# Performance work log

Measured on AMD Instinct MI355X. Metric: run time of the kernel, lower is better.

The kernel has to match this reference:

```python
import jax, jax.numpy as jnp
import numpy as np

B, S, V, K = 8, 128, 32000, 32


def setup_inputs() -> dict:
    key = jax.random.key(0)
    ks = jax.random.split(key, 8)
    return {
        "neural_logit": jax.random.normal(ks[0], (B, S, V), dtype=jnp.float32),
        "optor_vals": jax.random.randint(ks[1], (B, S, K), 0, V),
        "optor_dists": jax.random.uniform(ks[2], (B, S, K), dtype=jnp.float32) * 100.0,
        "const_vals": jax.random.randint(ks[3], (B, S, K), 0, V),
        "const_dists": jax.random.uniform(ks[4], (B, S, K), dtype=jnp.float32) * 100.0,
        "prev_words": jax.random.randint(ks[5], (B, S), 0, V),
        "optor_lamda": jnp.array([0.7], dtype=jnp.float32),
        "const_lamda": jnp.array([0.7], dtype=jnp.float32),
        "optor_temp": jnp.array([10.0], dtype=jnp.float32),
        "const_temp": jnp.array([10.0], dtype=jnp.float32),
    }


def _knn_prob(vals, dists, temp, vocab):
    # kernel-density: softmax over negative distances, scatter-add into vocab ids
    b, s, k = vals.shape
    w = jax.nn.softmax(-dists / temp, axis=-1)            # [B,S,K]
    rows = jnp.arange(b * s)[:, None]                     # [BS,1]
    p = jnp.zeros((b * s, vocab), w.dtype)
    p = p.at[rows, vals.reshape(b * s, k)].add(w.reshape(b * s, k))
    return p.reshape(b, s, vocab)


def reference(neural_logit, optor_vals, optor_dists, const_vals, const_dists,
              prev_words, optor_lamda, const_lamda, optor_temp, const_temp):
    nmt_prob = jax.nn.softmax(neural_logit, axis=-1)      # [B,S,V]

    optor_knn = _knn_prob(optor_vals, optor_dists, optor_temp[0], V)
    optor_combined = optor_lamda[0] * optor_knn + (1.0 - optor_lamda[0]) * nmt_prob

    const_knn = _knn_prob(const_vals, const_dists, const_temp[0], V)
    const_combined = const_lamda[0] * const_knn + (1.0 - const_lamda[0]) * nmt_prob

    pw = prev_words                                        # [B,S]
    optor_mask = (pw <= 88) | ((pw >= 91) & (pw <= 291))
    const_mask = (pw == 89) | (pw == 90) | (pw >= 292)

    combined = (optor_combined * optor_mask[:, :, None].astype(nmt_prob.dtype)
                + const_combined * const_mask[:, :, None].astype(nmt_prob.dtype))
    return combined
```

## Files before the change

kernel.cpp:

```cpp
#include <hip/hip_runtime.h>
#include <math.h>

constexpr int Bc = 8, Sc = 128, Vc = 32000, Kc = 32;
constexpr int NT = 1024;
constexpr int V4 = Vc / 4;
constexpr int ITERS = (V4 + NT - 1) / NT;
constexpr int NWAVES = NT / 64;

typedef float vfloat4 __attribute__((ext_vector_type(4)));

__global__ __launch_bounds__(NT) void SR_knnModel_kernel(
    const float* __restrict__ logit,
    const int*   __restrict__ optor_vals,
    const float* __restrict__ optor_dists,
    const int*   __restrict__ const_vals,
    const float* __restrict__ const_dists,
    const int*   __restrict__ prev_words,
    const float* __restrict__ optor_lamda,
    const float* __restrict__ const_lamda,
    const float* __restrict__ optor_temp,
    const float* __restrict__ const_temp,
    float* __restrict__ out)
{
    const int row = blockIdx.x;
    const int t   = threadIdx.x;
    const size_t base = (size_t)row * Vc;
    const float4* __restrict__ xin  = (const float4*)(logit + base);
    float* __restrict__        orow = out + base;

    float4 r[ITERS];
    float lmax = -INFINITY;
#pragma unroll
    for (int i = 0; i < ITERS; ++i) {
        const int idx = t + i * NT;
        if (i < ITERS - 1 || idx < V4) {
            const float4 v = xin[idx];
            r[i] = v;
            lmax = fmaxf(lmax, fmaxf(fmaxf(v.x, v.y), fmaxf(v.z, v.w)));
        }
    }

    float lsum = 0.f;
#pragma unroll
    for (int i = 0; i < ITERS; ++i) {
        const int idx = t + i * NT;
        if (i < ITERS - 1 || idx < V4) {
            float4 v = r[i];
            v.x = __expf(v.x - lmax);
            v.y = __expf(v.y - lmax);
            v.z = __expf(v.z - lmax);
            v.w = __expf(v.w - lmax);
            r[i] = v;
            lsum += (v.x + v.y) + (v.z + v.w);
        }
    }

    const int pw = prev_words[row];
    const float ol = optor_lamda[0];
    const float cl = const_lamda[0];

    float m = lmax, s = lsum;
#pragma unroll
    for (int off = 32; off > 0; off >>= 1) {
        const float om = __shfl_xor(m, off);
        const float os = __shfl_xor(s, off);
        const float M2 = fmaxf(m, om);
        s = s * __expf(m - M2) + os * __expf(om - M2);
        m = M2;
    }
    __shared__ float2 red[NWAVES];
    const int wave = t >> 6;
    if ((t & 63) == 0) red[wave] = make_float2(m, s);
    __syncthreads();
    float M = red[0].x, S = red[0].y;
#pragma unroll
    for (int w = 1; w < NWAVES; ++w) {
        const float2 p = red[w];
        const float nM = fmaxf(M, p.x);
        S = S * __expf(M - nM) + p.y * __expf(p.x - nM);
        M = nM;
    }

    const bool om_ = (pw <= 88) || (pw >= 91 && pw <= 291);
    const bool cm_ = (pw == 89) || (pw == 90) || (pw >= 292);
    const float omf = om_ ? 1.f : 0.f;
    const float cmf = cm_ ? 1.f : 0.f;
    const float cn = (1.f - ol) * omf + (1.f - cl) * cmf;
    const float f = __expf(lmax - M) * (cn / S);

#pragma unroll
    for (int i = 0; i < ITERS; ++i) {
        const int idx = t + i * NT;
        if (i < ITERS - 1 || idx < V4) {
            const float4 v = r[i];
            vfloat4 o;
            o.x = v.x * f; o.y = v.y * f; o.z = v.z * f; o.w = v.w * f;
            __builtin_nontemporal_store(o, (vfloat4*)orow + idx);
        }
    }
    __syncthreads();

    if (t < 32 || (t >= 64 && t < 96)) {
        const bool is_opt = (t < 32);
        const float scale = is_opt ? ol * omf : cl * cmf;
        if (scale != 0.f) {
            const int k = t & 31;
            const int*   vals  = is_opt ? optor_vals  : const_vals;
            const float* dists = is_opt ? optor_dists : const_dists;
            const float  temp  = is_opt ? optor_temp[0] : const_temp[0];
            const float sc = -dists[row * Kc + k] / temp;
            float mm = sc;
#pragma unroll
            for (int off = 16; off > 0; off >>= 1)
                mm = fmaxf(mm, __shfl_xor(mm, off));
            const float e = __expf(sc - mm);
            float sm = e;
#pragma unroll
            for (int off = 16; off > 0; off >>= 1)
                sm += __shfl_xor(sm, off);
            const float w = e / sm;
            atomicAdd(out + base + vals[row * Kc + k], scale * w);
        }
    }
}

extern "C" void kernel_launch(void* const* d_in, const int* in_sizes, int n_in,
                              void* d_out, int out_size, void* d_ws, size_t ws_size,
                              hipStream_t stream) {
    const float* logit       = (const float*)d_in[0];
    const int*   optor_vals  = (const int*)  d_in[1];
    const float* optor_dists = (const float*)d_in[2];
    const int*   const_vals  = (const int*)  d_in[3];
    const float* const_dists = (const float*)d_in[4];
    const int*   prev_words  = (const int*)  d_in[5];
    const float* optor_lamda = (const float*)d_in[6];
    const float* const_lamda = (const float*)d_in[7];
    const float* optor_temp  = (const float*)d_in[8];
    const float* const_temp  = (const float*)d_in[9];
    float* out = (float*)d_out;

    SR_knnModel_kernel<<<Bc * Sc, NT, 0, stream>>>(
        logit, optor_vals, optor_dists, const_vals, const_dists, prev_words,
        optor_lamda, const_lamda, optor_temp, const_temp, out);
}
```

Measured before the change: 249.8 us.

## Split softmax into row-statistics kernel and separate scale/write kernel

Splits the single fused row kernel into two launches. The first computes the per-row max and sum-of-exp and writes them to workspace. The second re-reads the logits with 256-thread blocks, recomputes exp and writes the scaled output plus the kNN scatter-add. This aims to drop the large register-resident row buffer in the write pass to improve occupancy, but it reads the 131 MB logit tensor twice, adds a second launch, and recomputes the exponentials.

```diff
diff --git a/kernel.cpp b/kernel.cpp
--- a/kernel.cpp
+++ b/kernel.cpp
@@ -2,15 +2,76 @@
 #include <math.h>
 
 constexpr int Bc = 8, Sc = 128, Vc = 32000, Kc = 32;
-constexpr int NT = 1024;
+constexpr int NROWS = Bc * Sc;
 constexpr int V4 = Vc / 4;
-constexpr int ITERS = (V4 + NT - 1) / NT;
-constexpr int NWAVES = NT / 64;
+
+constexpr int NTA = 1024;
+constexpr int ITA = (V4 + NTA - 1) / NTA;
+constexpr int NWA = NTA / 64;
+
+constexpr int NTB = 256;
+constexpr int ITB_FULL = V4 / NTB;
+constexpr int TAIL = V4 - ITB_FULL * NTB;
 
 typedef float vfloat4 __attribute__((ext_vector_type(4)));
 
-__global__ __launch_bounds__(NT) void SR_knnModel_kernel(
+__global__ __launch_bounds__(NTA) void SR_knn_rowstat(
     const float* __restrict__ logit,
+    float2* __restrict__ ws)
+{
+    const int row = blockIdx.x;
+    const int t   = threadIdx.x;
+    const float4* __restrict__ xin = (const float4*)(logit + (size_t)row * Vc);
+
+    float4 r[ITA];
+    float lmax = -INFINITY;
+#pragma unroll
+    for (int i = 0; i < ITA; ++i) {
+        const int idx = t + i * NTA;
+        if (i < ITA - 1 || idx < V4) {
+            const float4 v = xin[idx];
+            r[i] = v;
+            lmax = fmaxf(lmax, fmaxf(fmaxf(v.x, v.y), fmaxf(v.z, v.w)));
+        }
+    }
+    float lsum = 0.f;
+#pragma unroll
+    for (int i = 0; i < ITA; ++i) {
+        const int idx = t + i * NTA;
+        if (i < ITA - 1 || idx < V4) {
+            const float4 v = r[i];
+            lsum += (__expf(v.x - lmax) + __expf(v.y - lmax))
+                  + (__expf(v.z - lmax) + __expf(v.w - lmax));
+        }
+    }
+    float m = lmax, s = lsum;
+#pragma unroll
+    for (int off = 32; off > 0; off >>= 1) {
+        const float om = __shfl_xor(m, off);
+        const float os = __shfl_xor(s, off);
+        const float M2 = fmaxf(m, om);
+        s = s * __expf(m - M2) + os * __expf(om - M2);
+        m = M2;
+    }
+    __shared__ float2 red[NWA];
+    if ((t & 63) == 0) red[t >> 6] = make_float2(m, s);
+    __syncthreads();
+    if (t == 0) {
+        float M = red[0].x, S = red[0].y;
+#pragma unroll
+        for (int w = 1; w < NWA; ++w) {
+            const float2 p = red[w];
+            const float nM = fmaxf(M, p.x);
+            S = S * __expf(M - nM) + p.y * __expf(p.x - nM);
+            M = nM;
+        }
+        ws[row] = make_float2(M, S);
+    }
+}
+
+__global__ __launch_bounds__(NTB) void SR_knn_scale(
+    const float* __restrict__ logit,
+    const float2* __restrict__ ws,
     const int*   __restrict__ optor_vals,
     const float* __restrict__ optor_dists,
     const int*   __restrict__ const_vals,
@@ -28,75 +89,38 @@
     const float4* __restrict__ xin  = (const float4*)(logit + base);
     float* __restrict__        orow = out + base;
 
-    float4 r[ITERS];
-    float lmax = -INFINITY;
-#pragma unroll
-    for (int i = 0; i < ITERS; ++i) {
-        const int idx = t + i * NT;
-        if (i < ITERS - 1 || idx < V4) {
-            const float4 v = xin[idx];
-            r[i] = v;
-            lmax = fmaxf(lmax, fmaxf(fmaxf(v.x, v.y), fmaxf(v.z, v.w)));
-        }
-    }
-
-    float lsum = 0.f;
-#pragma unroll
-    for (int i = 0; i < ITERS; ++i) {
-        const int idx = t + i * NT;
-        if (i < ITERS - 1 || idx < V4) {
-            float4 v = r[i];
-            v.x = __expf(v.x - lmax);
-            v.y = __expf(v.y - lmax);
-            v.z = __expf(v.z - lmax);
-            v.w = __expf(v.w - lmax);
-            r[i] = v;
-            lsum += (v.x + v.y) + (v.z + v.w);
-        }
-    }
-
+    const float2 MS = ws[row];
     const int pw = prev_words[row];
     const float ol = optor_lamda[0];
     const float cl = const_lamda[0];
-
-    float m = lmax, s = lsum;
-#pragma unroll
-    for (int off = 32; off > 0; off >>= 1) {
-        const float om = __shfl_xor(m, off);
-        const float os = __shfl_xor(s, off);
-        const float M2 = fmaxf(m, om);
-        s = s * __expf(m - M2) + os * __expf(om - M2);
-        m = M2;
-    }
-    __shared__ float2 red[NWAVES];
-    const int wave = t >> 6;
-    if ((t & 63) == 0) red[wave] = make_float2(m, s);
-    __syncthreads();
-    float M = red[0].x, S = red[0].y;
-#pragma unroll
-    for (int w = 1; w < NWAVES; ++w) {
-        const float2 p = red[w];
-        const float nM = fmaxf(M, p.x);
-        S = S * __expf(M - nM) + p.y * __expf(p.x - nM);
-        M = nM;
-    }
-
     const bool om_ = (pw <= 88) || (pw >= 91 && pw <= 291);
     const bool cm_ = (pw == 89) || (pw == 90) || (pw >= 292);
     const float omf = om_ ? 1.f : 0.f;
     const float cmf = cm_ ? 1.f : 0.f;
     const float cn = (1.f - ol) * omf + (1.f - cl) * cmf;
-    const float f = __expf(lmax - M) * (cn / S);
+    const float M = MS.x;
+    const float f = cn / MS.y;
 
-#pragma unroll
-    for (int i = 0; i < ITERS; ++i) {
-        const int idx = t + i * NT;
-        if (i < ITERS - 1 || idx < V4) {
-            const float4 v = r[i];
-            vfloat4 o;
-            o.x = v.x * f; o.y = v.y * f; o.z = v.z * f; o.w = v.w * f;
-            __builtin_nontemporal_store(o, (vfloat4*)orow + idx);
-        }
+#pragma unroll 4
+    for (int i = 0; i < ITB_FULL; ++i) {
+        const int idx = t + i * NTB;
+        const float4 v = xin[idx];
+        vfloat4 o;
+        o.x = __expf(v.x - M) * f;
+        o.y = __expf(v.y - M) * f;
+        o.z = __expf(v.z - M) * f;
+        o.w = __expf(v.w - M) * f;
+        __builtin_nontemporal_store(o, (vfloat4*)orow + idx);
+    }
+    if (t < TAIL) {
+        const int idx = ITB_FULL * NTB + t;
+        const float4 v = xin[idx];
+        vfloat4 o;
+        o.x = __expf(v.x - M) * f;
+        o.y = __expf(v.y - M) * f;
+        o.z = __expf(v.z - M) * f;
+        o.w = __expf(v.w - M) * f;
+        __builtin_nontemporal_store(o, (vfloat4*)orow + idx);
     }
     __syncthreads();
 
@@ -138,8 +162,10 @@
     const float* optor_temp  = (const float*)d_in[8];
     const float* const_temp  = (const float*)d_in[9];
     float* out = (float*)d_out;
+    float2* stats = (float2*)d_ws;
 
-    SR_knnModel_kernel<<<Bc * Sc, NT, 0, stream>>>(
-        logit, optor_vals, optor_dists, const_vals, const_dists, prev_words,
-        optor_lamda, const_lamda, optor_temp, const_temp, out);
+    SR_knn_rowstat<<<NROWS, NTA, 0, stream>>>(logit, stats);
+    SR_knn_scale<<<NROWS, NTB, 0, stream>>>(
+        logit, stats, optor_vals, optor_dists, const_vals, const_dists,
+        prev_words, optor_lamda, const_lamda, optor_temp, const_temp, out);
 }
```

After: 265.3 us. 1.06x slower.

## Process four rows per block with register double-buffered prefetch, drop max subtraction

Applied to the files above, without the earlier changes.

Each block now handles four consecutive rows and prefetches the next row's logits into a second register buffer while the current row is normalised and stored, overlapping loads with stores and exp work. The online max reduction is removed and exp is taken on raw logits, which removes one reduction pass and its exp rescaling but can overflow for large logits. The grid shrinks by a factor of four and register pressure roughly doubles, which may reduce occupancy. kNN scatter is done by one wave per row after all four rows are written.

```diff
diff --git a/kernel.cpp b/kernel.cpp
--- a/kernel.cpp
+++ b/kernel.cpp
@@ -2,10 +2,13 @@
 #include <math.h>
 
 constexpr int Bc = 8, Sc = 128, Vc = 32000, Kc = 32;
+constexpr int NROWS = Bc * Sc;
+constexpr int V4 = Vc / 4;
 constexpr int NT = 1024;
-constexpr int V4 = Vc / 4;
-constexpr int ITERS = (V4 + NT - 1) / NT;
-constexpr int NWAVES = NT / 64;
+constexpr int IT = (V4 + NT - 1) / NT;
+constexpr int NW = NT / 64;
+constexpr int RPB = 4;
+constexpr int GRID = NROWS / RPB;
 
 typedef float vfloat4 __attribute__((ext_vector_type(4)));
 
@@ -22,89 +25,115 @@
     const float* __restrict__ const_temp,
     float* __restrict__ out)
 {
-    const int row = blockIdx.x;
-    const int t   = threadIdx.x;
-    const size_t base = (size_t)row * Vc;
-    const float4* __restrict__ xin  = (const float4*)(logit + base);
-    float* __restrict__        orow = out + base;
+    const int t    = threadIdx.x;
+    const int wave = t >> 6;
+    const int row0 = blockIdx.x * RPB;
 
-    float4 r[ITERS];
-    float lmax = -INFINITY;
+    __shared__ float red[2][NW];
+
+    const float ol = optor_lamda[0];
+    const float cl = const_lamda[0];
+
+    float4 bufA[IT], bufB[IT];
+    float lsum = 0.f;
+
+    {
+        const float4* __restrict__ xin = (const float4*)(logit + (size_t)row0 * Vc);
 #pragma unroll
-    for (int i = 0; i < ITERS; ++i) {
-        const int idx = t + i * NT;
-        if (i < ITERS - 1 || idx < V4) {
-            const float4 v = xin[idx];
-            r[i] = v;
-            lmax = fmaxf(lmax, fmaxf(fmaxf(v.x, v.y), fmaxf(v.z, v.w)));
+        for (int i = 0; i < IT; ++i) {
+            const int idx = t + i * NT;
+            if (i < IT - 1 || idx < V4) bufA[i] = xin[idx];
+        }
+#pragma unroll
+        for (int i = 0; i < IT; ++i) {
+            const int idx = t + i * NT;
+            if (i < IT - 1 || idx < V4) {
+                float4 v = bufA[i];
+                v.x = __expf(v.x); v.y = __expf(v.y);
+                v.z = __expf(v.z); v.w = __expf(v.w);
+                bufA[i] = v;
+                lsum += (v.x + v.y) + (v.z + v.w);
+            }
         }
     }
 
-    float lsum = 0.f;
+    auto stage = [&](float4 (&cur)[IT], float4 (&nxt)[IT], const int j) {
+        const int row = row0 + j;
+
+        float s = lsum;
 #pragma unroll
-    for (int i = 0; i < ITERS; ++i) {
-        const int idx = t + i * NT;
-        if (i < ITERS - 1 || idx < V4) {
-            float4 v = r[i];
-            v.x = __expf(v.x - lmax);
-            v.y = __expf(v.y - lmax);
-            v.z = __expf(v.z - lmax);
-            v.w = __expf(v.w - lmax);
-            r[i] = v;
-            lsum += (v.x + v.y) + (v.z + v.w);
+        for (int off = 32; off > 0; off >>= 1)
+            s += __shfl_xor(s, off);
+        if ((t & 63) == 0) red[j & 1][wave] = s;
+        asm volatile("s_waitcnt lgkmcnt(0)\n\ts_barrier" ::: "memory");
+        __builtin_amdgcn_sched_barrier(0);
+        float S = 0.f;
+#pragma unroll
+        for (int w = 0; w < NW; ++w) S += red[j & 1][w];
+
+        const int pw = prev_words[row];
+        const bool om_ = (pw <= 88) || (pw >= 91 && pw <= 291);
+        const bool cm_ = (pw == 89) || (pw == 90) || (pw >= 292);
+        const float cn = (1.f - ol) * (om_ ? 1.f : 0.f)
+                       + (1.f - cl) * (cm_ ? 1.f : 0.f);
+        const float f = cn / S;
+
+        if (j + 1 < RPB) {
+            const float4* __restrict__ xin =
+                (const float4*)(logit + (size_t)(row + 1) * Vc);
+#pragma unroll
+            for (int i = 0; i < IT; ++i) {
+                const int idx = t + i * NT;
+                if (i < IT - 1 || idx < V4) nxt[i] = xin[idx];
+            }
         }
-    }
 
-    const int pw = prev_words[row];
-    const float ol = optor_lamda[0];
-    const float cl = const_lamda[0];
+        float* __restrict__ orow = out + (size_t)row * Vc;
+#pragma unroll
+        for (int i = 0; i < IT; ++i) {
+            const int idx = t + i * NT;
+            if (i < IT - 1 || idx < V4) {
+                const float4 v = cur[i];
+                vfloat4 o;
+                o.x = v.x * f; o.y = v.y * f; o.z = v.z * f; o.w = v.w * f;
+                __builtin_nontemporal_store(o, (vfloat4*)orow + idx);
+            }
+        }
 
-    float m = lmax, s = lsum;
+        if (j + 1 < RPB) {
+            lsum = 0.f;
 #pragma unroll
-    for (int off = 32; off > 0; off >>= 1) {
-        const float om = __shfl_xor(m, off);
-        const float os = __shfl_xor(s, off);
-        const float M2 = fmaxf(m, om);
-        s = s * __expf(m - M2) + os * __expf(om - M2);
-        m = M2;
-    }
-    __shared__ float2 red[NWAVES];
-    const int wave = t >> 6;
-    if ((t & 63) == 0) red[wave] = make_float2(m, s);
-    __syncthreads();
-    float M = red[0].x, S = red[0].y;
-#pragma unroll
-    for (int w = 1; w < NWAVES; ++w) {
-        const float2 p = red[w];
-        const float nM = fmaxf(M, p.x);
-        S = S * __expf(M - nM) + p.y * __expf(p.x - nM);
-        M = nM;
-    }
+            for (int i = 0; i < IT; ++i) {
+                const int idx = t + i * NT;
+                if (i < IT - 1 || idx < V4) {
+                    float4 v = nxt[i];
+                    v.x = __expf(v.x); v.y = __expf(v.y);
+                    v.z = __expf(v.z); v.w = __expf(v.w);
+                    nxt[i] = v;
+                    lsum += (v.x + v.y) + (v.z + v.w);
+                }
+            }
+        }
+    };
 
-    const bool om_ = (pw <= 88) || (pw >= 91 && pw <= 291);
-    const bool cm_ = (pw == 89) || (pw == 90) || (pw >= 292);
-    const float omf = om_ ? 1.f : 0.f;
-    const float cmf = cm_ ? 1.f : 0.f;
-    const float cn = (1.f - ol) * omf + (1.f - cl) * cmf;
-    const float f = __expf(lmax - M) * (cn / S);
+    stage(bufA, bufB, 0);
+    stage(bufB, bufA, 1);
+    stage(bufA, bufB, 2);
+    stage(bufB, bufA, 3);
 
-#pragma unroll
-    for (int i = 0; i < ITERS; ++i) {
-        const int idx = t + i * NT;
-        if (i < ITERS - 1 || idx < V4) {
-            const float4 v = r[i];
-            vfloat4 o;
-            o.x = v.x * f; o.y = v.y * f; o.z = v.z * f; o.w = v.w * f;
-            __builtin_nontemporal_store(o, (vfloat4*)orow + idx);
-        }
-    }
     __syncthreads();
 
-    if (t < 32 || (t >= 64 && t < 96)) {
-        const bool is_opt = (t < 32);
-        const float scale = is_opt ? ol * omf : cl * cmf;
+    if (wave < RPB) {
+        const int row  = row0 + wave;
+        const int lane = t & 63;
+        const bool is_opt = lane < 32;
+        const int k = lane & 31;
+        const int pw = prev_words[row];
+        const bool om_ = (pw <= 88) || (pw >= 91 && pw <= 291);
+        const bool cm_ = (pw == 89) || (pw == 90) || (pw >= 292);
+        const float scale = is_opt ? ol * (om_ ? 1.f : 0.f)
+                                   : cl * (cm_ ? 1.f : 0.f);
         if (scale != 0.f) {
-            const int k = t & 31;
             const int*   vals  = is_opt ? optor_vals  : const_vals;
             const float* dists = is_opt ? optor_dists : const_dists;
             const float  temp  = is_opt ? optor_temp[0] : const_temp[0];
@@ -118,8 +147,8 @@
 #pragma unroll
             for (int off = 16; off > 0; off >>= 1)
                 sm += __shfl_xor(sm, off);
-            const float w = e / sm;
-            atomicAdd(out + base + vals[row * Kc + k], scale * w);
+            atomicAdd(out + (size_t)row * Vc + vals[row * Kc + k],
+                      scale * (e / sm));
         }
     }
 }
@@ -139,7 +168,7 @@
     const float* const_temp  = (const float*)d_in[9];
     float* out = (float*)d_out;
 
-    SR_knnModel_kernel<<<Bc * Sc, NT, 0, stream>>>(
+    SR_knnModel_kernel<<<GRID, NT, 0, stream>>>(
         logit, optor_vals, optor_dists, const_vals, const_dists, prev_words,
         optor_lamda, const_lamda, optor_temp, const_temp, out);
 }
```

Measured after the change: 250.9 us. Within noise of the previous version (+0.5%).
